# Kernel tuning notes

Measured on AMD Instinct MI355X. Metric: run time of the kernel, lower is better.

Reference implementation:

```python
import jax, jax.numpy as jnp
import numpy as np

D_EQUI = 64
D_INV = 256
D_MSG = 64
N_HEADS = 32
D_HEAD = D_INV // N_HEADS
D_FF = 256
D_EDGE_IN = 64
D_EDGE_OUT = 64
D_OUT = D_EQUI + N_HEADS + D_EDGE_OUT  # 160
IN_FEATS = 2 * D_MSG + D_EQUI + D_EDGE_IN  # 256
B, N = 4, 256


def setup_inputs() -> dict:
    key = jax.random.key(0)
    ks = jax.random.split(key, 20)
    s = 0.05
    inp = {
        "equis": jax.random.normal(ks[0], (B, N, 3, D_EQUI), jnp.float32),
        "invs": jax.random.normal(ks[1], (B, N, D_INV), jnp.float32),
        "edges": jax.random.normal(ks[2], (B, N, N, D_EDGE_IN), jnp.float32),
        "adj_matrix": jnp.ones((B, N, N), jnp.int32),
        # _PairwiseMessages params
        "qW": jax.random.normal(ks[3], (D_INV, D_MSG), jnp.float32) * s,
        "qb": jnp.zeros((D_MSG,), jnp.float32),
        "kW": jax.random.normal(ks[4], (D_INV, D_MSG), jnp.float32) * s,
        "kb": jnp.zeros((D_MSG,), jnp.float32),
        "mW1": jax.random.normal(ks[5], (IN_FEATS, D_FF), jnp.float32) * s,
        "mb1": jnp.zeros((D_FF,), jnp.float32),
        "mW2": jax.random.normal(ks[6], (D_FF, D_OUT), jnp.float32) * s,
        "mb2": jnp.zeros((D_OUT,), jnp.float32),
        # _InvAttention params
        "inv_inW": jax.random.normal(ks[7], (D_INV, D_INV), jnp.float32) * s,
        "inv_inb": jnp.zeros((D_INV,), jnp.float32),
        "inv_outW": jax.random.normal(ks[8], (D_INV, D_INV), jnp.float32) * s,
        "inv_outb": jnp.zeros((D_INV,), jnp.float32),
        # _EquiAttention params (no bias)
        "equi_inW": jax.random.normal(ks[9], (D_EQUI, D_EQUI), jnp.float32) * s,
        "equi_outW": jax.random.normal(ks[10], (D_EQUI, D_EQUI), jnp.float32) * s,
    }
    return inp


def _forward(equis, invs, edges, adj_matrix, qW, qb, kW, kb, mW1, mb1, mW2, mb2,
             inv_inW, inv_inb, inv_outW, inv_outb, equi_inW, equi_outW):
    # ---- pairwise messages ----
    # dotprods of equivariant 3-vectors per channel: [B, Nq, Nk, d_equi]
    dot = jnp.einsum("bqdc,bkdc->bqkc", equis, equis)
    qm = invs @ qW + qb  # [B,N,d_msg]
    km = invs @ kW + kb
    Nn = invs.shape[1]
    feats = jnp.concatenate([
        jnp.broadcast_to(qm[:, :, None, :], (qm.shape[0], Nn, Nn, D_MSG)),
        jnp.broadcast_to(km[:, None, :, :], (km.shape[0], Nn, Nn, D_MSG)),
        dot,
        edges,
    ], axis=-1)  # [B,N,N,in_feats]
    msgs = jax.nn.silu(feats @ mW1 + mb1) @ mW2 + mb2  # [B,N,N,d_out]

    # adjacency -> additive mask (0 where connected, -inf otherwise)
    mask = jnp.where(adj_matrix == 0, -jnp.inf, 0.0).astype(msgs.dtype)

    # ---- invariant attention (first n_heads channels) ----
    inv_msgs = msgs[..., :N_HEADS] + mask[..., None]
    attn_i = jax.nn.softmax(inv_msgs, axis=2)  # softmax over kv
    hf = (invs @ inv_inW + inv_inb).reshape(invs.shape[0], Nn, N_HEADS, D_HEAD)
    out_i = jnp.einsum("bqkh,bkhd->bqhd", attn_i, hf)
    w_i = jnp.sqrt(jnp.sum(attn_i * attn_i, axis=2))  # [B,q,H]
    out_i = out_i * w_i[..., None]
    inv_updates = out_i.reshape(invs.shape[0], Nn, D_INV) @ inv_outW + inv_outb

    # ---- equivariant attention (next d_equi channels) ----
    equi_msgs = msgs[..., N_HEADS:N_HEADS + D_EQUI] + mask[..., None]
    attn_e = jax.nn.softmax(equi_msgs, axis=2)  # [B,q,k,c]
    pe = equis @ equi_inW  # [B,N,3,d_equi]
    out_e = jnp.einsum("bqkc,bkdc->bqdc", attn_e, pe)
    w_e = jnp.sqrt(jnp.sum(attn_e * attn_e, axis=2))  # [B,q,c]
    out_e = out_e * w_e[:, :, None, :]
    equi_updates = out_e @ equi_outW  # [B,N,3,d_equi]

    # ---- edge updates (remaining channels) ----
    edge_updates = msgs[..., N_HEADS + D_EQUI:]
    return equi_updates, inv_updates, edge_updates


def reference(equis, invs, edges, adj_matrix, qW, qb, kW, kb, mW1, mb1, mW2, mb2,
              inv_inW, inv_inb, inv_outW, inv_outb, equi_inW, equi_outW):
    return _forward(equis, invs, edges, adj_matrix, qW, qb, kW, kb, mW1, mb1, mW2, mb2,
                    inv_inW, inv_inb, inv_outW, inv_outb, equi_inW, equi_outW)
```

## Files before the change

kernel.cpp:

```cpp
#include <hip/hip_runtime.h>
#include <hip/hip_bf16.h>
#include <math.h>


typedef __attribute__((ext_vector_type(8))) short short8;
typedef __attribute__((ext_vector_type(8))) __bf16 bf16x8;
typedef __attribute__((ext_vector_type(4))) float f32x4;

constexpr int EQUI_OFF = 0;
constexpr int INV_OFF  = 196608;
constexpr int EDGE_OFF = 458752;

__device__ __forceinline__ unsigned short f2bf(float x) {
    unsigned u = __builtin_bit_cast(unsigned, x);
    u = u + 0x7FFFu + ((u >> 16) & 1u);
    return (unsigned short)(u >> 16);
}
__device__ __forceinline__ float bf2f(unsigned short u) {
    return __builtin_bit_cast(float, ((unsigned)u) << 16);
}
__device__ __forceinline__ unsigned short f2bfh(float x) {
    return __builtin_bit_cast(unsigned short, (__bf16)x);
}
__device__ __forceinline__ short8 pk8(f32x4 a, f32x4 b) {
    bf16x8 r = { (__bf16)a.x, (__bf16)a.y, (__bf16)a.z, (__bf16)a.w,
                 (__bf16)b.x, (__bf16)b.y, (__bf16)b.z, (__bf16)b.w };
    return __builtin_bit_cast(short8, r);
}
__device__ __forceinline__ f32x4 MFMA(short8 a, short8 b, f32x4 c) {
    return __builtin_amdgcn_mfma_f32_16x16x32_bf16(
        __builtin_bit_cast(bf16x8, a), __builtin_bit_cast(bf16x8, b), c, 0, 0, 0);
}

__global__ void prep_weights(const float* __restrict__ mW1, const float* __restrict__ mW2,
                             short* __restrict__ W1T, short* __restrict__ W2T) {
    int idx = blockIdx.x * 256 + threadIdx.x;
    if (idx < 49152) {
        int n = idx / 192, kk = idx - n * 192;
        int row = (kk < 128) ? (128 + kk) : (kk - 64);
        W1T[idx] = (short)f2bf(mW1[row * 256 + n]);
    } else {
        int i2 = idx - 49152;
        int n = i2 >> 8, f = i2 & 255;
        W2T[i2] = (short)f2bf(mW2[f * 160 + n]);
    }
}

__global__ void prep_proj(const float* __restrict__ invs, const float* __restrict__ equis,
                          const float* __restrict__ qW, const float* __restrict__ qb,
                          const float* __restrict__ kW, const float* __restrict__ kb,
                          const float* __restrict__ inv_inW, const float* __restrict__ inv_inb,
                          const float* __restrict__ equi_inW,
                          float* __restrict__ qm, float* __restrict__ km,
                          float* __restrict__ hf, float* __restrict__ pe) {
    int tid = threadIdx.x;
    if (blockIdx.x < 1024) {
        int r = blockIdx.x;
        __shared__ float sInv[256];
        sInv[tid] = invs[r * 256 + tid];
        __syncthreads();
        if (tid < 64) {
            float acc = qb[tid];
            for (int f = 0; f < 256; ++f) acc += sInv[f] * qW[f * 64 + tid];
            qm[r * 64 + tid] = acc;
        } else if (tid < 128) {
            int c = tid - 64;
            float acc = kb[c];
            for (int f = 0; f < 256; ++f) acc += sInv[f] * kW[f * 64 + c];
            km[r * 64 + c] = acc;
        }
        float acch = inv_inb[tid];
        for (int f = 0; f < 256; ++f) acch += sInv[f] * inv_inW[f * 256 + tid];
        hf[r * 256 + tid] = acch;
    } else {
        int rn = blockIdx.x - 1024;
        if (tid < 192) {
            int d = tid >> 6, c = tid & 63;
            const float* erow = equis + (size_t)rn * 192 + d * 64;
            float acc = 0.f;
            for (int f = 0; f < 64; ++f) acc += erow[f] * equi_inW[f * 64 + c];
            pe[rn * 192 + d * 64 + c] = acc;
        }
    }
}

__global__ void prep_c1(const float* __restrict__ qm, const float* __restrict__ mW1,
                        const float* __restrict__ mb1, float* __restrict__ c1) {
    int tid = threadIdx.x, r = blockIdx.x;
    __shared__ float s[64];
    if (tid < 64) s[tid] = qm[r * 64 + tid];
    __syncthreads();
    float acc = mb1[tid];
    #pragma unroll 8
    for (int k = 0; k < 64; ++k) acc = fmaf(s[k], mW1[k * 256 + tid], acc);
    c1[r * 256 + tid] = acc;
}

__global__ void prep_T(const float* __restrict__ hf, const float* __restrict__ pe,
                       const float* __restrict__ inv_outW, const float* __restrict__ equi_outW,
                       unsigned short* __restrict__ hfT, unsigned short* __restrict__ peT,
                       unsigned short* __restrict__ WoT, unsigned short* __restrict__ EoT) {
    __shared__ float sT[64][65];
    int tid = threadIdx.x, bi = blockIdx.x;
    if (bi < 64) {
        int b = bi >> 4, t = bi & 15, tj = t >> 2, th = t & 3;
        #pragma unroll
        for (int i = 0; i < 16; ++i) { int idx = i * 256 + tid; int jl = idx >> 6, hl = idx & 63;
            sT[jl][hl] = hf[((size_t)(b * 256 + tj * 64 + jl)) * 256 + th * 64 + hl]; }
        __syncthreads();
        #pragma unroll
        for (int i = 0; i < 16; ++i) { int idx = i * 256 + tid; int hl = idx >> 6, jl = idx & 63;
            hfT[((size_t)(b * 256 + th * 64 + hl)) * 256 + tj * 64 + jl] = f2bf(sT[jl][hl]); }
    } else if (bi < 128) {
        int i2 = bi - 64; int b = i2 >> 4, t = i2 & 15, tj = t >> 2, d = t & 3;
        if (d == 3) {
            #pragma unroll
            for (int i = 0; i < 16; ++i) { int idx = i * 256 + tid; int c = idx >> 6, jl = idx & 63;
                peT[((size_t)((b * 64 + c) * 4 + 3)) * 256 + tj * 64 + jl] = 0; }
        } else {
            #pragma unroll
            for (int i = 0; i < 16; ++i) { int idx = i * 256 + tid; int jl = idx >> 6, c = idx & 63;
                sT[jl][c] = pe[((size_t)(b * 256 + tj * 64 + jl)) * 192 + d * 64 + c]; }
            __syncthreads();
            #pragma unroll
            for (int i = 0; i < 16; ++i) { int idx = i * 256 + tid; int c = idx >> 6, jl = idx & 63;
                peT[((size_t)((b * 64 + c) * 4 + d)) * 256 + tj * 64 + jl] = f2bf(sT[jl][c]); }
        }
    } else if (bi < 144) {
        int i2 = bi - 128; int tf = i2 >> 2, tn = i2 & 3;
        #pragma unroll
        for (int i = 0; i < 16; ++i) { int idx = i * 256 + tid; int fl = idx >> 6, nl = idx & 63;
            sT[fl][nl] = inv_outW[(size_t)(tf * 64 + fl) * 256 + tn * 64 + nl]; }
        __syncthreads();
        #pragma unroll
        for (int i = 0; i < 16; ++i) { int idx = i * 256 + tid; int nl = idx >> 6, fl = idx & 63;
            WoT[(size_t)(tn * 64 + nl) * 256 + tf * 64 + fl] = f2bf(sT[fl][nl]); }
    } else {
        #pragma unroll
        for (int i = 0; i < 16; ++i) { int idx = i * 256 + tid; int cl = idx >> 6, c2 = idx & 63;
            sT[cl][c2] = equi_outW[cl * 64 + c2]; }
        __syncthreads();
        #pragma unroll
        for (int i = 0; i < 16; ++i) { int idx = i * 256 + tid; int c2 = idx >> 6, cl = idx & 63;
            EoT[c2 * 64 + cl] = f2bf(sT[cl][c2]); }
    }
}

constexpr int GA_AH   = 0;
constexpr int GA_EQ   = 32768;
constexpr int GA_MASK = 33536;
constexpr int GA_BYTES = 33792;

__launch_bounds__(256, 4)
__global__ void semla_gemm(const float* __restrict__ equis, const float* __restrict__ edges,
                           const int* __restrict__ adj, const float* __restrict__ mb2,
                           const short* __restrict__ W1T, const short* __restrict__ W2T,
                           const float* __restrict__ c1, const float* __restrict__ km,
                           float* __restrict__ out, unsigned short* __restrict__ PT) {
    extern __shared__ char smem[];
    float* sEQ   = (float*)(smem + GA_EQ);
    float* sMask = (float*)(smem + GA_MASK);

    const int tid  = threadIdx.x;
    const int lane = tid & 63;
    const int w    = tid >> 6;
    const int bid  = blockIdx.x;
    const int bq   = bid >> 2;
    const int jc   = bid & 3;
    const int b    = bq >> 8;

    const int lrow = lane & 15;
    const int kgrp = (lane >> 4) << 3;
    const int drow = (lane >> 4) << 2;

    if (tid < 192) sEQ[tid] = equis[(size_t)bq * 192 + tid];
    if (tid < 64)  sMask[tid] = adj[(size_t)bq * 256 + (jc << 6) + tid] ? 0.f : -1e30f;

    float c1v[4];
    #pragma unroll
    for (int ni = 0; ni < 4; ++ni)
        c1v[ni] = c1[bq * 256 + (w << 6) + (ni << 4) + lrow];

    auto stA16 = [&](int row, int colbyte, short8 v) {
        int byte = (row * 384 + colbyte) ^ ((row & 7) << 4);
        *(short8*)(smem + GA_AH + byte) = v;
    };
    auto ldA = [&](int row, int kb) -> short8 {
        int byte = (row * 384 + (kb << 1)) ^ ((row & 7) << 4);
        return *(const short8*)(smem + GA_AH + byte);
    };
    auto stH = [&](int row, int col, unsigned short v) {
        int byte = ((row << 9) + (col << 1)) ^ ((row & 7) << 4);
        *(unsigned short*)(smem + GA_AH + byte) = v;
    };
    auto ldH = [&](int row, int kb) -> short8 {
        int byte = ((row << 9) + (kb << 1)) ^ ((row & 7) << 4);
        return *(const short8*)(smem + GA_AH + byte);
    };

    __syncthreads();

    {
        int r = tid >> 2, h = tid & 3;
        const float* erow = equis + (size_t)((b << 8) + (jc << 6) + r) * 192;
        #pragma unroll
        for (int g = 0; g < 2; ++g) {
            int cg = h + g * 4;
            f32x4 lo = (f32x4)(0.f), hi = (f32x4)(0.f);
            #pragma unroll
            for (int d = 0; d < 3; ++d) {
                f32x4 e0 = *(const f32x4*)(erow + d * 64 + cg * 8);
                f32x4 e1 = *(const f32x4*)(erow + d * 64 + cg * 8 + 4);
                f32x4 q0 = *(const f32x4*)(sEQ + d * 64 + cg * 8);
                f32x4 q1 = *(const f32x4*)(sEQ + d * 64 + cg * 8 + 4);
                lo += e0 * q0; hi += e1 * q1;
            }
            stA16(r, cg * 16, pk8(lo, hi));
        }
        const float* ebase = edges + ((size_t)bq * 256 + (jc << 6)) * 64;
        const float* kbase = km + (size_t)((b << 8) + (jc << 6)) * 64;
        #pragma unroll
        for (int it = 0; it < 2; ++it) {
            int id = it * 256 + tid;
            int rr = id >> 3, c8 = id & 7;
            f32x4 e0 = *(const f32x4*)(ebase + rr * 64 + c8 * 8);
            f32x4 e1 = *(const f32x4*)(ebase + rr * 64 + c8 * 8 + 4);
            stA16(rr, 128 + c8 * 16, pk8(e0, e1));
            f32x4 k0 = *(const f32x4*)(kbase + rr * 64 + c8 * 8);
            f32x4 k1 = *(const f32x4*)(kbase + rr * 64 + c8 * 8 + 4);
            stA16(rr, 256 + c8 * 16, pk8(k0, k1));
        }
    }
    __syncthreads();

    f32x4 acc[4][4];
    #pragma unroll
    for (int mi = 0; mi < 4; ++mi)
        #pragma unroll
        for (int ni = 0; ni < 4; ++ni) acc[mi][ni] = (f32x4)(0.f);

    #pragma unroll
    for (int k0 = 0; k0 < 192; k0 += 32) {
        int kb = k0 + kgrp;
        short8 a0 = ldA(lrow, kb), a1 = ldA(16 + lrow, kb),
               a2 = ldA(32 + lrow, kb), a3 = ldA(48 + lrow, kb);
        short8 bf[4];
        #pragma unroll
        for (int ni = 0; ni < 4; ++ni)
            bf[ni] = *(const short8*)(W1T + ((w << 6) + (ni << 4) + lrow) * 192 + kb);
        #pragma unroll
        for (int ni = 0; ni < 4; ++ni) {
            acc[0][ni] = MFMA(a0, bf[ni], acc[0][ni]);
            acc[1][ni] = MFMA(a1, bf[ni], acc[1][ni]);
            acc[2][ni] = MFMA(a2, bf[ni], acc[2][ni]);
            acc[3][ni] = MFMA(a3, bf[ni], acc[3][ni]);
        }
    }
    __syncthreads();

    #pragma unroll
    for (int mi = 0; mi < 4; ++mi)
        #pragma unroll
        for (int r = 0; r < 4; ++r) {
            int row = (mi << 4) + drow + r;
            #pragma unroll
            for (int ni = 0; ni < 4; ++ni) {
                int n = (w << 6) + (ni << 4) + lrow;
                float x = acc[mi][ni][r] + c1v[ni];
                float hh = x * __builtin_amdgcn_rcpf(1.f + __expf(-x));
                stH(row, n, f2bfh(hh));
            }
        }
    __syncthreads();

    if (w < 2) {
        float b2v[3][4];
        #pragma unroll
        for (int tn = 0; tn < 3; ++tn)
            #pragma unroll
            for (int r = 0; r < 4; ++r)
                b2v[tn][r] = mb2[w * 48 + tn * 16 + drow + r];
        float mj[4];
        #pragma unroll
        for (int tj = 0; tj < 4; ++tj) mj[tj] = sMask[tj * 16 + lrow];

        f32x4 acc2[3][4];
        #pragma unroll
        for (int tn = 0; tn < 3; ++tn)
            #pragma unroll
            for (int tj = 0; tj < 4; ++tj) acc2[tn][tj] = (f32x4)(0.f);

        #pragma unroll
        for (int k0 = 0; k0 < 256; k0 += 32) {
            int kb = k0 + kgrp;
            short8 hB[4];
            #pragma unroll
            for (int tj = 0; tj < 4; ++tj) hB[tj] = ldH(tj * 16 + lrow, kb);
            #pragma unroll
            for (int tn = 0; tn < 3; ++tn) {
                short8 wA = *(const short8*)(W2T + (w * 48 + tn * 16 + lrow) * 256 + kb);
                #pragma unroll
                for (int tj = 0; tj < 4; ++tj)
                    acc2[tn][tj] = MFMA(wA, hB[tj], acc2[tn][tj]);
            }
        }
        unsigned short* ptbase = PT + (((size_t)bq * 96) << 8) + (jc << 6);
        #pragma unroll
        for (int tn = 0; tn < 3; ++tn)
            #pragma unroll
            for (int tj = 0; tj < 4; ++tj)
                #pragma unroll
                for (int r = 0; r < 4; ++r) {
                    int n2 = w * 48 + tn * 16 + drow + r;
                    float v = acc2[tn][tj][r] + b2v[tn][r] + mj[tj];
                    ptbase[((size_t)n2 << 8) + tj * 16 + lrow] = f2bfh(v);
                }
    } else {
        const int nb = 96 + (w - 2) * 32;
        float b2v[2];
        #pragma unroll
        for (int ti = 0; ti < 2; ++ti) b2v[ti] = mb2[nb + ti * 16 + lrow];

        f32x4 acc2[4][2];
        #pragma unroll
        for (int mi = 0; mi < 4; ++mi)
            #pragma unroll
            for (int ti = 0; ti < 2; ++ti) acc2[mi][ti] = (f32x4)(0.f);

        #pragma unroll
        for (int k0 = 0; k0 < 256; k0 += 32) {
            int kb = k0 + kgrp;
            short8 a0 = ldH(lrow, kb), a1 = ldH(16 + lrow, kb),
                   a2 = ldH(32 + lrow, kb), a3 = ldH(48 + lrow, kb);
            #pragma unroll
            for (int ti = 0; ti < 2; ++ti) {
                short8 bb = *(const short8*)(W2T + (nb + ti * 16 + lrow) * 256 + kb);
                acc2[0][ti] = MFMA(a0, bb, acc2[0][ti]);
                acc2[1][ti] = MFMA(a1, bb, acc2[1][ti]);
                acc2[2][ti] = MFMA(a2, bb, acc2[2][ti]);
                acc2[3][ti] = MFMA(a3, bb, acc2[3][ti]);
            }
        }
        #pragma unroll
        for (int mi = 0; mi < 4; ++mi)
            #pragma unroll
            for (int ti = 0; ti < 2; ++ti) {
                int n = nb + ti * 16 + lrow;
                #pragma unroll
                for (int r = 0; r < 4; ++r) {
                    int j = (jc << 6) + (mi << 4) + drow + r;
                    out[EDGE_OFF + ((size_t)bq * 256 + j) * 64 + (n - 96)] = acc2[mi][ti][r] + b2v[ti];
                }
            }
    }
}

constexpr int ES_A = 0;
constexpr int ES_W = 32768;
constexpr int ES_BYTES = 33024;

__launch_bounds__(256, 4)
__global__ void semla_einsum(const unsigned short* __restrict__ PT,
                             const unsigned short* __restrict__ hfT,
                             const unsigned short* __restrict__ peT,
                             unsigned short* __restrict__ OIb, unsigned short* __restrict__ OEb) {
    extern __shared__ char smem[];
    float* sW = (float*)(smem + ES_W);
    const int tid = threadIdx.x, lane = tid & 63, w = tid >> 6;
    const int bi = blockIdx.x;
    const int qc = bi & 3;
    const int t  = bi >> 2;
    const int b  = t / 96;
    const int c  = t - 96 * b;
    const int lrow = lane & 15, kgrp = (lane >> 4) << 3, drow = (lane >> 4) << 2;

    #pragma unroll
    for (int i = 0; i < 8; ++i) {
        int id = i * 256 + tid; int row = id >> 5, ck = id & 31;
        size_t src = (((size_t)((b << 8) + (qc << 6) + row) * 96 + c) << 8) + ck * 16;
        short8 v = *(const short8*)(PT + src);
        int byte = ((row << 9) + (ck << 4)) ^ ((row & 7) << 4);
        *(short8*)(smem + ES_A + byte) = v;
    }
    __syncthreads();

    {
        int r = tid >> 2, p = tid & 3;
        float v[64];
        #pragma unroll
        for (int i = 0; i < 8; ++i) {
            int ck = p * 8 + i;
            int byte = ((r << 9) + (ck << 4)) ^ ((r & 7) << 4);
            short8 x = *(const short8*)(smem + ES_A + byte);
            #pragma unroll
            for (int e = 0; e < 8; ++e) v[i * 8 + e] = bf2f((unsigned short)x[e]);
        }
        float m = v[0];
        #pragma unroll
        for (int i = 1; i < 64; ++i) m = fmaxf(m, v[i]);
        m = fmaxf(m, __shfl_xor(m, 1)); m = fmaxf(m, __shfl_xor(m, 2));
        float s = 0.f, q = 0.f;
        #pragma unroll
        for (int i = 0; i < 64; ++i) { float e = __expf(v[i] - m); v[i] = e; s += e; q = fmaf(e, e, q); }
        s += __shfl_xor(s, 1); s += __shfl_xor(s, 2);
        q += __shfl_xor(q, 1); q += __shfl_xor(q, 2);
        float rs = (s > 0.f) ? 1.f / s : 0.f;
        if (p == 0) sW[r] = sqrtf(q) * rs;
        #pragma unroll
        for (int i = 0; i < 8; ++i) {
            int ck = p * 8 + i;
            short8 o;
            #pragma unroll
            for (int e = 0; e < 8; ++e) o[e] = (short)f2bfh(v[i * 8 + e] * rs);
            int byte = ((r << 9) + (ck << 4)) ^ ((r & 7) << 4);
            *(short8*)(smem + ES_A + byte) = o;
        }
    }
    __syncthreads();

    const unsigned short* Bbase =
        (c < 32) ? hfT + (((size_t)((b << 8) + (c << 3) + (lrow & 7))) << 8)
                 : peT + (((size_t)((((b << 6) + (c - 32)) << 2) + (lrow & 3))) << 8);
    f32x4 acc = (f32x4)(0.f);
    #pragma unroll
    for (int k0 = 0; k0 < 256; k0 += 32) {
        int kb = k0 + kgrp;
        int byte = ((((w << 4) + lrow) << 9) + (kb << 1)) ^ ((lrow & 7) << 4);
        short8 a = *(const short8*)(smem + ES_A + byte);
        short8 bb = *(const short8*)(Bbase + kb);
        acc = MFMA(a, bb, acc);
    }
    const int nvalid = (c < 32) ? 8 : 3;
    if (lrow < nvalid) {
        #pragma unroll
        for (int r2 = 0; r2 < 4; ++r2) {
            int ql = (w << 4) + drow + r2;
            float val = acc[r2] * sW[ql];
            size_t grow = (size_t)((b << 8) + (qc << 6) + ql);
            if (c < 32) OIb[(grow << 8) + (c << 3) + lrow] = f2bfh(val);
            else        OEb[(grow * 3 + lrow) * 64 + (c - 32)] = f2bfh(val);
        }
    }
}

constexpr int PJ_BYTES = 32768;

__launch_bounds__(256, 4)
__global__ void semla_proj(const unsigned short* __restrict__ OIb,
                           const unsigned short* __restrict__ OEb,
                           const unsigned short* __restrict__ WoT,
                           const unsigned short* __restrict__ EoT,
                           const float* __restrict__ inv_outb, float* __restrict__ out) {
    extern __shared__ char smem[];
    const int tid = threadIdx.x, lane = tid & 63, w = tid >> 6;
    const int lrow = lane & 15, kgrp = (lane >> 4) << 3, drow = (lane >> 4) << 2;
    const int bi = blockIdx.x;

    if (bi < 32) {
        const int mb = bi >> 1, nb = bi & 1;
        #pragma unroll
        for (int i = 0; i < 8; ++i) {
            int id = i * 256 + tid; int row = id >> 5, ck = id & 31;
            short8 v = *(const short8*)(OIb + (((size_t)(mb * 64 + row)) << 8) + ck * 16);
            int byte = ((row << 9) + (ck << 4)) ^ ((row & 7) << 4);
            *(short8*)(smem + byte) = v;
        }
        __syncthreads();
        f32x4 acc[4][2];
        #pragma unroll
        for (int mi = 0; mi < 4; ++mi)
            #pragma unroll
            for (int ti = 0; ti < 2; ++ti) acc[mi][ti] = (f32x4)(0.f);
        #pragma unroll
        for (int k0 = 0; k0 < 256; k0 += 32) {
            int kb = k0 + kgrp;
            short8 a[4];
            #pragma unroll
            for (int mi = 0; mi < 4; ++mi) {
                int byte = ((((mi << 4) + lrow) << 9) + (kb << 1)) ^ ((lrow & 7) << 4);
                a[mi] = *(const short8*)(smem + byte);
            }
            #pragma unroll
            for (int ti = 0; ti < 2; ++ti) {
                int n = nb * 128 + w * 32 + (ti << 4) + lrow;
                short8 bb = *(const short8*)(WoT + n * 256 + kb);
                #pragma unroll
                for (int mi = 0; mi < 4; ++mi) acc[mi][ti] = MFMA(a[mi], bb, acc[mi][ti]);
            }
        }
        #pragma unroll
        for (int ti = 0; ti < 2; ++ti) {
            int n = nb * 128 + w * 32 + (ti << 4) + lrow;
            float bias = inv_outb[n];
            #pragma unroll
            for (int mi = 0; mi < 4; ++mi)
                #pragma unroll
                for (int r = 0; r < 4; ++r) {
                    int row = mb * 64 + (mi << 4) + drow + r;
                    out[INV_OFF + (size_t)row * 256 + n] = acc[mi][ti][r] + bias;
                }
        }
    } else {
        const int mb = bi - 32;
        #pragma unroll
        for (int i = 0; i < 2; ++i) {
            int id = i * 256 + tid; int row = id >> 3, ck = id & 7;
            short8 v = *(const short8*)(OEb + (((size_t)(mb * 64 + row)) << 6) + ck * 16);
            int byte = ((row << 7) + (ck << 4)) ^ ((row & 7) << 4);
            *(short8*)(smem + byte) = v;
        }
        __syncthreads();
        f32x4 acc[4];
        #pragma unroll
        for (int ni = 0; ni < 4; ++ni) acc[ni] = (f32x4)(0.f);
        #pragma unroll
        for (int k0 = 0; k0 < 64; k0 += 32) {
            int kb = k0 + kgrp;
            int byte = ((((w << 4) + lrow) << 7) + (kb << 1)) ^ ((lrow & 7) << 4);
            short8 a = *(const short8*)(smem + byte);
            #pragma unroll
            for (int ni = 0; ni < 4; ++ni) {
                short8 bb = *(const short8*)(EoT + ((ni << 4) + lrow) * 64 + kb);
                acc[ni] = MFMA(a, bb, acc[ni]);
            }
        }
        #pragma unroll
        for (int ni = 0; ni < 4; ++ni)
            #pragma unroll
            for (int r = 0; r < 4; ++r) {
                int rowg = mb * 64 + (w << 4) + drow + r;
                int bq = rowg / 3, d = rowg - 3 * bq;
                out[EQUI_OFF + (size_t)bq * 192 + d * 64 + (ni << 4) + lrow] = acc[ni][r];
            }
    }
}

extern "C" void kernel_launch(void* const* d_in, const int* in_sizes, int n_in,
                              void* d_out, int out_size, void* d_ws, size_t ws_size,
                              hipStream_t stream) {
    const float* equis    = (const float*)d_in[0];
    const float* invs     = (const float*)d_in[1];
    const float* edges    = (const float*)d_in[2];
    const int*   adj      = (const int*)d_in[3];
    const float* qW       = (const float*)d_in[4];
    const float* qb       = (const float*)d_in[5];
    const float* kW       = (const float*)d_in[6];
    const float* kb       = (const float*)d_in[7];
    const float* mW1      = (const float*)d_in[8];
    const float* mb1      = (const float*)d_in[9];
    const float* mW2      = (const float*)d_in[10];
    const float* mb2      = (const float*)d_in[11];
    const float* inv_inW  = (const float*)d_in[12];
    const float* inv_inb  = (const float*)d_in[13];
    const float* inv_outW = (const float*)d_in[14];
    const float* inv_outb = (const float*)d_in[15];
    const float* equi_inW = (const float*)d_in[16];
    const float* equi_outW= (const float*)d_in[17];

    char* ws = (char*)d_ws;
    short* W1T = (short*)(ws + 0);
    short* W2T = (short*)(ws + 98304);
    float* qm  = (float*)(ws + 180224);
    float* km  = (float*)(ws + 442368);
    float* hf  = (float*)(ws + 704512);
    float* pe  = (float*)(ws + 1753088);
    float* c1  = (float*)(ws + 2539520);
    unsigned short* hfT = (unsigned short*)(ws + 3588096);
    unsigned short* peT = (unsigned short*)(ws + 4112384);
    unsigned short* OIb = (unsigned short*)(ws + 4636672);
    unsigned short* OEb = (unsigned short*)(ws + 5160960);
    unsigned short* WoT = (unsigned short*)(ws + 5554176);
    unsigned short* EoT = (unsigned short*)(ws + 5685248);
    unsigned short* PT  = (unsigned short*)(ws + 5693440);

    prep_weights<<<352, 256, 0, stream>>>(mW1, mW2, W1T, W2T);
    prep_proj<<<2048, 256, 0, stream>>>(invs, equis, qW, qb, kW, kb,
                                        inv_inW, inv_inb, equi_inW, qm, km, hf, pe);
    prep_c1<<<1024, 256, 0, stream>>>(qm, mW1, mb1, c1);
    prep_T<<<145, 256, 0, stream>>>(hf, pe, inv_outW, equi_outW, hfT, peT, WoT, EoT);
    semla_gemm<<<4096, 256, GA_BYTES, stream>>>(equis, edges, adj, mb2, W1T, W2T,
                                                c1, km, (float*)d_out, PT);
    semla_einsum<<<1536, 256, ES_BYTES, stream>>>(PT, hfT, peT, OIb, OEb);
    semla_proj<<<80, 256, PJ_BYTES, stream>>>(OIb, OEb, WoT, EoT, inv_outb, (float*)d_out);
}
```

Baseline: 171.6 us.

## Halve gemm row tile to 32 and stage PT output through shared memory

Result: slower. 246.2 us (+43.5%).

```diff
diff --git a/kernel.cpp b/kernel.cpp
--- a/kernel.cpp
+++ b/kernel.cpp
@@ -147,11 +147,11 @@
 }
 
 constexpr int GA_AH   = 0;
-constexpr int GA_EQ   = 32768;
-constexpr int GA_MASK = 33536;
-constexpr int GA_BYTES = 33792;
-
-__launch_bounds__(256, 4)
+constexpr int GA_EQ   = 16384;
+constexpr int GA_MASK = 17152;
+constexpr int GA_BYTES = 17280;
+
+__launch_bounds__(256, 5)
 __global__ void semla_gemm(const float* __restrict__ equis, const float* __restrict__ edges,
                            const int* __restrict__ adj, const float* __restrict__ mb2,
                            const short* __restrict__ W1T, const short* __restrict__ W2T,
@@ -165,8 +165,8 @@
     const int lane = tid & 63;
     const int w    = tid >> 6;
     const int bid  = blockIdx.x;
-    const int bq   = bid >> 2;
-    const int jc   = bid & 3;
+    const int bq   = bid >> 3;
+    const int jb   = (bid & 7) << 5;
     const int b    = bq >> 8;
 
     const int lrow = lane & 15;
@@ -174,7 +174,7 @@
     const int drow = (lane >> 4) << 2;
 
     if (tid < 192) sEQ[tid] = equis[(size_t)bq * 192 + tid];
-    if (tid < 64)  sMask[tid] = adj[(size_t)bq * 256 + (jc << 6) + tid] ? 0.f : -1e30f;
+    if (tid < 32)  sMask[tid] = adj[(size_t)bq * 256 + jb + tid] ? 0.f : -1e30f;
 
     float c1v[4];
     #pragma unroll
@@ -201,49 +201,39 @@
     __syncthreads();
 
     {
-        int r = tid >> 2, h = tid & 3;
-        const float* erow = equis + (size_t)((b << 8) + (jc << 6) + r) * 192;
-        #pragma unroll
-        for (int g = 0; g < 2; ++g) {
-            int cg = h + g * 4;
-            f32x4 lo = (f32x4)(0.f), hi = (f32x4)(0.f);
-            #pragma unroll
-            for (int d = 0; d < 3; ++d) {
-                f32x4 e0 = *(const f32x4*)(erow + d * 64 + cg * 8);
-                f32x4 e1 = *(const f32x4*)(erow + d * 64 + cg * 8 + 4);
-                f32x4 q0 = *(const f32x4*)(sEQ + d * 64 + cg * 8);
-                f32x4 q1 = *(const f32x4*)(sEQ + d * 64 + cg * 8 + 4);
-                lo += e0 * q0; hi += e1 * q1;
-            }
-            stA16(r, cg * 16, pk8(lo, hi));
-        }
-        const float* ebase = edges + ((size_t)bq * 256 + (jc << 6)) * 64;
-        const float* kbase = km + (size_t)((b << 8) + (jc << 6)) * 64;
-        #pragma unroll
-        for (int it = 0; it < 2; ++it) {
-            int id = it * 256 + tid;
-            int rr = id >> 3, c8 = id & 7;
-            f32x4 e0 = *(const f32x4*)(ebase + rr * 64 + c8 * 8);
-            f32x4 e1 = *(const f32x4*)(ebase + rr * 64 + c8 * 8 + 4);
-            stA16(rr, 128 + c8 * 16, pk8(e0, e1));
-            f32x4 k0 = *(const f32x4*)(kbase + rr * 64 + c8 * 8);
-            f32x4 k1 = *(const f32x4*)(kbase + rr * 64 + c8 * 8 + 4);
-            stA16(rr, 256 + c8 * 16, pk8(k0, k1));
-        }
-    }
-    __syncthreads();
-
-    f32x4 acc[4][4];
+        int r = tid >> 3, h = tid & 7;
+        const float* erow = equis + (size_t)((b << 8) + jb + r) * 192;
+        f32x4 lo = (f32x4)(0.f), hi = (f32x4)(0.f);
+        #pragma unroll
+        for (int d = 0; d < 3; ++d) {
+            f32x4 e0 = *(const f32x4*)(erow + d * 64 + h * 8);
+            f32x4 e1 = *(const f32x4*)(erow + d * 64 + h * 8 + 4);
+            f32x4 q0 = *(const f32x4*)(sEQ + d * 64 + h * 8);
+            f32x4 q1 = *(const f32x4*)(sEQ + d * 64 + h * 8 + 4);
+            lo += e0 * q0; hi += e1 * q1;
+        }
+        stA16(r, h * 16, pk8(lo, hi));
+        const float* ebase = edges + ((size_t)bq * 256 + jb) * 64;
+        const float* kbase = km + (size_t)((b << 8) + jb) * 64;
+        f32x4 e0 = *(const f32x4*)(ebase + r * 64 + h * 8);
+        f32x4 e1 = *(const f32x4*)(ebase + r * 64 + h * 8 + 4);
+        stA16(r, 128 + h * 16, pk8(e0, e1));
+        f32x4 k0 = *(const f32x4*)(kbase + r * 64 + h * 8);
+        f32x4 k1 = *(const f32x4*)(kbase + r * 64 + h * 8 + 4);
+        stA16(r, 256 + h * 16, pk8(k0, k1));
+    }
+    __syncthreads();
+
+    f32x4 acc[2][4];
     #pragma unroll
-    for (int mi = 0; mi < 4; ++mi)
+    for (int mi = 0; mi < 2; ++mi)
         #pragma unroll
         for (int ni = 0; ni < 4; ++ni) acc[mi][ni] = (f32x4)(0.f);
 
     #pragma unroll
     for (int k0 = 0; k0 < 192; k0 += 32) {
         int kb = k0 + kgrp;
-        short8 a0 = ldA(lrow, kb), a1 = ldA(16 + lrow, kb),
-               a2 = ldA(32 + lrow, kb), a3 = ldA(48 + lrow, kb);
+        short8 a0 = ldA(lrow, kb), a1 = ldA(16 + lrow, kb);
         short8 bf[4];
         #pragma unroll
         for (int ni = 0; ni < 4; ++ni)
@@ -252,14 +242,12 @@
         for (int ni = 0; ni < 4; ++ni) {
             acc[0][ni] = MFMA(a0, bf[ni], acc[0][ni]);
             acc[1][ni] = MFMA(a1, bf[ni], acc[1][ni]);
-            acc[2][ni] = MFMA(a2, bf[ni], acc[2][ni]);
-            acc[3][ni] = MFMA(a3, bf[ni], acc[3][ni]);
         }
     }
     __syncthreads();
 
     #pragma unroll
-    for (int mi = 0; mi < 4; ++mi)
+    for (int mi = 0; mi < 2; ++mi)
         #pragma unroll
         for (int r = 0; r < 4; ++r) {
             int row = (mi << 4) + drow + r;
@@ -280,78 +268,83 @@
             #pragma unroll
             for (int r = 0; r < 4; ++r)
                 b2v[tn][r] = mb2[w * 48 + tn * 16 + drow + r];
-        float mj[4];
-        #pragma unroll
-        for (int tj = 0; tj < 4; ++tj) mj[tj] = sMask[tj * 16 + lrow];
-
-        f32x4 acc2[3][4];
+        float mj0 = sMask[lrow], mj1 = sMask[16 + lrow];
+
+        f32x4 acc2[3][2];
         #pragma unroll
         for (int tn = 0; tn < 3; ++tn)
             #pragma unroll
-            for (int tj = 0; tj < 4; ++tj) acc2[tn][tj] = (f32x4)(0.f);
+            for (int tj = 0; tj < 2; ++tj) acc2[tn][tj] = (f32x4)(0.f);
 
         #pragma unroll
         for (int k0 = 0; k0 < 256; k0 += 32) {
             int kb = k0 + kgrp;
-            short8 hB[4];
-            #pragma unroll
-            for (int tj = 0; tj < 4; ++tj) hB[tj] = ldH(tj * 16 + lrow, kb);
+            short8 hB0 = ldH(lrow, kb), hB1 = ldH(16 + lrow, kb);
             #pragma unroll
             for (int tn = 0; tn < 3; ++tn) {
                 short8 wA = *(const short8*)(W2T + (w * 48 + tn * 16 + lrow) * 256 + kb);
-                #pragma unroll
-                for (int tj = 0; tj < 4; ++tj)
-                    acc2[tn][tj] = MFMA(wA, hB[tj], acc2[tn][tj]);
-            }
-        }
-        unsigned short* ptbase = PT + (((size_t)bq * 96) << 8) + (jc << 6);
+                acc2[tn][0] = MFMA(wA, hB0, acc2[tn][0]);
+                acc2[tn][1] = MFMA(wA, hB1, acc2[tn][1]);
+            }
+        }
+        __syncthreads();
         #pragma unroll
         for (int tn = 0; tn < 3; ++tn)
             #pragma unroll
-            for (int tj = 0; tj < 4; ++tj)
+            for (int tj = 0; tj < 2; ++tj) {
+                float mj = tj ? mj1 : mj0;
                 #pragma unroll
                 for (int r = 0; r < 4; ++r) {
                     int n2 = w * 48 + tn * 16 + drow + r;
-                    float v = acc2[tn][tj][r] + b2v[tn][r] + mj[tj];
-                    ptbase[((size_t)n2 << 8) + tj * 16 + lrow] = f2bfh(v);
+                    int j  = tj * 16 + lrow;
+                    float v = acc2[tn][tj][r] + b2v[tn][r] + mj;
+                    *(unsigned short*)(smem + n2 * 72 + j * 2) = f2bfh(v);
                 }
+            }
     } else {
         const int nb = 96 + (w - 2) * 32;
         float b2v[2];
         #pragma unroll
         for (int ti = 0; ti < 2; ++ti) b2v[ti] = mb2[nb + ti * 16 + lrow];
 
-        f32x4 acc2[4][2];
-        #pragma unroll
-        for (int mi = 0; mi < 4; ++mi)
+        f32x4 acc2[2][2];
+        #pragma unroll
+        for (int mi = 0; mi < 2; ++mi)
             #pragma unroll
             for (int ti = 0; ti < 2; ++ti) acc2[mi][ti] = (f32x4)(0.f);
 
         #pragma unroll
         for (int k0 = 0; k0 < 256; k0 += 32) {
             int kb = k0 + kgrp;
-            short8 a0 = ldH(lrow, kb), a1 = ldH(16 + lrow, kb),
-                   a2 = ldH(32 + lrow, kb), a3 = ldH(48 + lrow, kb);
+            short8 a0 = ldH(lrow, kb), a1 = ldH(16 + lrow, kb);
             #pragma unroll
             for (int ti = 0; ti < 2; ++ti) {
                 short8 bb = *(const short8*)(W2T + (nb + ti * 16 + lrow) * 256 + kb);
                 acc2[0][ti] = MFMA(a0, bb, acc2[0][ti]);
                 acc2[1][ti] = MFMA(a1, bb, acc2[1][ti]);
-                acc2[2][ti] = MFMA(a2, bb, acc2[2][ti]);
-                acc2[3][ti] = MFMA(a3, bb, acc2[3][ti]);
-            }
-        }
-        #pragma unroll
-        for (int mi = 0; mi < 4; ++mi)
+            }
+        }
+        __syncthreads();
+        #pragma unroll
+        for (int mi = 0; mi < 2; ++mi)
             #pragma unroll
             for (int ti = 0; ti < 2; ++ti) {
                 int n = nb + ti * 16 + lrow;
                 #pragma unroll
                 for (int r = 0; r < 4; ++r) {
-                    int j = (jc << 6) + (mi << 4) + drow + r;
+                    int j = jb + (mi << 4) + drow + r;
                     out[EDGE_OFF + ((size_t)bq * 256 + j) * 64 + (n - 96)] = acc2[mi][ti][r] + b2v[ti];
                 }
             }
+    }
+    __syncthreads();
+
+    if (tid < 192) {
+        int n = tid >> 1, half = tid & 1;
+        const char* src = smem + n * 72 + half * 32;
+        unsigned short* dst = PT + (((size_t)bq * 96 + n) << 8) + jb + half * 16;
+        *(short8*)(dst)     = *(const short8*)(src);
+        *(short8*)(dst + 8) = *(const short8*)(src + 16);
     }
 }
 
@@ -578,7 +571,7 @@
                                         inv_inW, inv_inb, equi_inW, qm, km, hf, pe);
     prep_c1<<<1024, 256, 0, stream>>>(qm, mW1, mb1, c1);
     prep_T<<<145, 256, 0, stream>>>(hf, pe, inv_outW, equi_outW, hfT, peT, WoT, EoT);
-    semla_gemm<<<4096, 256, GA_BYTES, stream>>>(equis, edges, adj, mb2, W1T, W2T,
+    semla_gemm<<<8192, 256, GA_BYTES, stream>>>(equis, edges, adj, mb2, W1T, W2T,
                                                 c1, km, (float*)d_out, PT);
     semla_einsum<<<1536, 256, ES_BYTES, stream>>>(PT, hfT, peT, OIb, OEb);
     semla_proj<<<80, 256, PJ_BYTES, stream>>>(OIb, OEb, WoT, EoT, inv_outb, (float*)d_out);
```
